# Performance work log

Measured on AMD Instinct MI355X. Metric: run time of the kernel, lower is better.

The kernel has to match this reference:

```python
import jax, jax.numpy as jnp
import numpy as np

PATCH = 16; D = 384; HEADS = 6; HD = D // HEADS; DEPTH = 12
NUM_CH = 64; MAXY = 4000  # (max_sr//2)*max_win_size
THETA = 100.0; EPS = 1e-6
WIN_SHIFT_FACTOR = 0.25; MIN_WIN_SHIFT = 0.125  # min_win_size*win_shift_factor


def _layer_norm(x, g, b):
    mu = jnp.mean(x, -1, keepdims=True)
    var = jnp.mean((x - mu) ** 2, -1, keepdims=True)
    return (x - mu) * jax.lax.rsqrt(var + EPS) * g + b


def _rope(t, cos, sin):
    # t: [B,H,N,HD]; cos/sin: [N,HD//2]; consecutive-pair complex rotation
    shp = t.shape
    tr = t.reshape(shp[:-1] + (HD // 2, 2))
    a, b = tr[..., 0], tr[..., 1]
    return jnp.stack([a * cos - b * sin, a * sin + b * cos], axis=-1).reshape(shp)


def _forward(x, means, stds, channels, noise, win_size, mask_ratio,
             patch_w, patch_b, cls_token, chan_table, mean_w, mean_b,
             qkv_w, qkv_b, proj_w, proj_b, fc1_w, fc1_b, fc2_w, fc2_b,
             ln1_g, ln1_b, ln2_g, ln2_b, gamma1, gamma2, lnf_g, lnf_b):
    B = x.shape[0]
    # --- patch embed (conv k=s=16) ---
    feat = jax.lax.conv_general_dilated(x, patch_w, (PATCH, PATCH), 'VALID',
                                        dimension_numbers=('NCHW', 'OIHW', 'NCHW'))
    h, w = feat.shape[2], feat.shape[3]
    N = h * w
    xt = feat.reshape(B, D, N).transpose(0, 2, 1) + patch_b  # [B,N,D]
    # --- vectorized channel-id embedding lookup (replaces BxN python loop) ---
    xt = xt + chan_table[channels]
    # --- normalization meta patches (original uses mean_embed for BOTH means and stds) ---
    m = means @ mean_w + mean_b
    s = stds @ mean_w + mean_b
    norm_patches = jnp.concatenate([m, s], axis=2)  # [B,M,D]
    M = norm_patches.shape[1]
    xt = jnp.concatenate([norm_patches, xt], axis=1)
    xt = jnp.concatenate([jnp.broadcast_to(cls_token, (B, 1, D)), xt], axis=1)
    n_meta = M + 1
    meta_patches = xt[:, :n_meta]
    # --- random masking (meta tokens always kept) ---
    data = xt[:, n_meta:]
    Ld = data.shape[1]
    len_keep = int(Ld * (1 - mask_ratio))
    ids_shuffle = jnp.argsort(noise, axis=1)
    ids_restore = jnp.argsort(ids_shuffle, axis=1)
    kept = jnp.take_along_axis(data, ids_shuffle[:, :len_keep, None], axis=1)
    mask0 = jnp.broadcast_to((jnp.arange(Ld) >= len_keep).astype(xt.dtype), (B, Ld))
    mask = jnp.take_along_axis(mask0, ids_restore, axis=1)
    xt = jnp.concatenate([xt[:, :n_meta], kept], axis=1)
    # --- axial RoPE freqs for the current hxw patch grid ---
    step = float(win_size) * WIN_SHIFT_FACTOR / MIN_WIN_SHIFT
    nf = HD // 4
    inv = 1.0 / (THETA ** (jnp.arange(0, HD, 4)[:nf].astype(jnp.float32) / HD))
    ys, xs = jnp.meshgrid(jnp.arange(h, dtype=jnp.float32),
                          jnp.arange(w, dtype=jnp.float32) * step, indexing='ij')
    fr = jnp.concatenate([xs.reshape(-1, 1) * inv, ys.reshape(-1, 1) * inv], axis=-1)  # [N,HD//2]
    cos, sin = jnp.cos(fr), jnp.sin(fr)
    # --- layer-scale RoPE transformer blocks ---
    L = xt.shape[1]
    scale = HD ** -0.5
    for d in range(DEPTH):
        y = _layer_norm(xt, ln1_g[d], ln1_b[d])
        qkv = (y @ qkv_w[d] + qkv_b[d]).reshape(B, L, 3, HEADS, HD).transpose(2, 0, 3, 1, 4)
        q, k, v = qkv[0], qkv[1], qkv[2]
        q = jnp.concatenate([q[:, :, :n_meta], _rope(q[:, :, n_meta:], cos, sin)], axis=2)
        k = jnp.concatenate([k[:, :, :n_meta], _rope(k[:, :, n_meta:], cos, sin)], axis=2)
        a = jax.nn.softmax(jnp.einsum('bhqd,bhkd->bhqk', q, k) * scale, axis=-1)
        o = jnp.einsum('bhqk,bhkd->bhqd', a, v).transpose(0, 2, 1, 3).reshape(B, L, D)
        xt = xt + gamma1[d] * (o @ proj_w[d] + proj_b[d])
        y2 = _layer_norm(xt, ln2_g[d], ln2_b[d])
        hid = jax.nn.gelu(y2 @ fc1_w[d] + fc1_b[d], approximate=False)
        xt = xt + gamma2[d] * (hid @ fc2_w[d] + fc2_b[d])
    xt = _layer_norm(xt, lnf_g, lnf_b)
    return xt, meta_patches, mask, n_meta


def setup_inputs() -> dict:
    key = jax.random.key(0)
    ks = jax.random.split(key, 16)
    B, H, W, M = 4, 128, 1024, 2
    N = (H // PATCH) * (W // PATCH)
    nrm = lambda k, shp, s=0.02: jax.random.normal(k, shp, jnp.float32) * s
    inp = {}
    inp['x'] = jax.random.normal(ks[0], (B, 1, H, W), jnp.float32)
    inp['means'] = jax.random.normal(ks[1], (B, M, MAXY), jnp.float32) * 0.1
    inp['stds'] = jax.random.normal(ks[2], (B, M, MAXY), jnp.float32) * 0.1
    inp['channels'] = jax.random.randint(ks[3], (B, N), 0, NUM_CH, jnp.int32)
    inp['noise'] = jnp.broadcast_to(jnp.arange(N, dtype=jnp.float32), (B, N))  # identity shuffle
    inp['win_size'] = 2
    inp['mask_ratio'] = 0
    inp['patch_w'] = nrm(ks[4], (D, 1, PATCH, PATCH))
    inp['patch_b'] = jnp.zeros((D,), jnp.float32)
    inp['cls_token'] = jnp.zeros((1, 1, D), jnp.float32)
    inp['chan_table'] = nrm(ks[5], (NUM_CH, D))
    inp['mean_w'] = nrm(ks[6], (MAXY, D // 2), 0.01)
    inp['mean_b'] = jnp.zeros((D // 2,), jnp.float32)
    inp['qkv_w'] = nrm(ks[7], (DEPTH, D, 3 * D))
    inp['qkv_b'] = jnp.zeros((DEPTH, 3 * D), jnp.float32)
    inp['proj_w'] = nrm(ks[8], (DEPTH, D, D))
    inp['proj_b'] = jnp.zeros((DEPTH, D), jnp.float32)
    inp['fc1_w'] = nrm(ks[9], (DEPTH, D, 4 * D))
    inp['fc1_b'] = jnp.zeros((DEPTH, 4 * D), jnp.float32)
    inp['fc2_w'] = nrm(ks[10], (DEPTH, 4 * D, D))
    inp['fc2_b'] = jnp.zeros((DEPTH, D), jnp.float32)
    inp['ln1_g'] = jnp.ones((DEPTH, D), jnp.float32)
    inp['ln1_b'] = jnp.zeros((DEPTH, D), jnp.float32)
    inp['ln2_g'] = jnp.ones((DEPTH, D), jnp.float32)
    inp['ln2_b'] = jnp.zeros((DEPTH, D), jnp.float32)
    inp['gamma1'] = jnp.full((DEPTH, D), 1e-4, jnp.float32)
    inp['gamma2'] = jnp.full((DEPTH, D), 1e-4, jnp.float32)
    inp['lnf_g'] = jnp.ones((D,), jnp.float32)
    inp['lnf_b'] = jnp.zeros((D,), jnp.float32)
    return inp


def reference(x, means, stds, channels, noise, win_size, mask_ratio,
              patch_w, patch_b, cls_token, chan_table, mean_w, mean_b,
              qkv_w, qkv_b, proj_w, proj_b, fc1_w, fc1_b, fc2_w, fc2_b,
              ln1_g, ln1_b, ln2_g, ln2_b, gamma1, gamma2, lnf_g, lnf_b):
    return _forward(x, means, stds, channels, noise, win_size, mask_ratio,
                    patch_w, patch_b, cls_token, chan_table, mean_w, mean_b,
                    qkv_w, qkv_b, proj_w, proj_b, fc1_w, fc1_b, fc2_w, fc2_b,
                    ln1_g, ln1_b, ln2_g, ln2_b, gamma1, gamma2, lnf_g, lnf_b)
```

## Files before the change

### kernel.cpp

```cpp
#include <hip/hip_runtime.h>
#include <hip/hip_bf16.h>
#include <math.h>

#define Bq     4
#define LSEQ   515
#define NMETA  3
#define NPATCH 512
#define Dm     384
#define NHEADS 6
#define HDh    64
#define NDEPTH 12
#define LPAD   544
#define KSPL   32
#define KCH    125

typedef unsigned short u16;
typedef short bf16x8 __attribute__((ext_vector_type(8)));
typedef float f32x4  __attribute__((ext_vector_type(4)));

enum { EPI_F32 = 0, EPI_BF16 = 1, EPI_GELU = 2, EPI_RES = 3 };

__device__ inline u16 f2bf(float x) {
    __hip_bfloat16 h = __float2bfloat16(x);
    return *reinterpret_cast<u16*>(&h);
}
__device__ inline float bf2f(u16 x) {
    __hip_bfloat16 h = *reinterpret_cast<__hip_bfloat16*>(&x);
    return __bfloat162float(h);
}

__global__ __launch_bounds__(256)
void k_transpose(const float* __restrict__ W, u16* __restrict__ WT, int R, int C) {
    __shared__ float tile[32][33];
    int z = blockIdx.z;
    const float* Wz = W + (long)z * R * C;
    u16* Tz = WT + (long)z * R * C;
    int c0 = blockIdx.x * 32, r0 = blockIdx.y * 32;
    int tx = threadIdx.x & 31, ty = threadIdx.x >> 5;
    for (int rr = ty; rr < 32; rr += 8)
        tile[rr][tx] = Wz[(long)(r0 + rr) * C + c0 + tx];
    __syncthreads();
    for (int rr = ty; rr < 32; rr += 8)
        Tz[(long)(c0 + rr) * R + r0 + tx] = f2bf(tile[tx][rr]);
}

__global__ __launch_bounds__(256)
void k_split(const float* __restrict__ x, u16* __restrict__ A) {
    int m = blockIdx.x;
    int b = m >> 9, n = m & 511;
    int i = n >> 6, j = n & 63;
    int t = threadIdx.x;
    int pr = t >> 4, pc = t & 15;
    float v = x[(long)b * 131072 + (i * 16 + pr) * 1024 + j * 16 + pc];
    u16 hi = f2bf(v);
    u16 lo = f2bf(v - bf2f(hi));
    u16* row = A + (long)m * 768;
    row[t] = hi; row[256 + t] = hi; row[512 + t] = lo;
}

__global__ __launch_bounds__(256)
void k_wsplit(const float* __restrict__ pw, u16* __restrict__ Bt) {
    int idx = blockIdx.x * 256 + threadIdx.x;
    if (idx >= Dm * 256) return;
    int d = idx >> 8, k = idx & 255;
    float v = pw[idx];
    u16 hi = f2bf(v);
    u16 lo = f2bf(v - bf2f(hi));
    u16* row = Bt + (long)d * 768;
    row[k] = hi; row[256 + k] = lo; row[512 + k] = hi;
}

__global__ __launch_bounds__(512)
void k_argsort(const float* __restrict__ noise, int* __restrict__ ids) {
    __shared__ float v[512];
    __shared__ int   ix[512];
    int b = blockIdx.x, t = threadIdx.x;
    v[t] = noise[b * 512 + t]; ix[t] = t;
    __syncthreads();
    for (int k = 2; k <= 512; k <<= 1)
        for (int j = k >> 1; j > 0; j >>= 1) {
            int p = t ^ j;
            if (p > t) {
                bool up = (t & k) == 0;
                float va = v[t], vb = v[p]; int ia = ix[t], ib = ix[p];
                bool sw = (va > vb) || (va == vb && ia > ib);
                if (sw == up) { v[t] = vb; v[p] = va; ix[t] = ib; ix[p] = ia; }
            }
            __syncthreads();
        }
    ids[b * 512 + t] = ix[t];
}

__global__ void k_gather(const float* __restrict__ tmp, const int* __restrict__ ids,
                         const float* __restrict__ pb, const float* __restrict__ ctab,
                         const int* __restrict__ chan, float* __restrict__ xt) {
    long t = (long)blockIdx.x * 256 + threadIdx.x;
    if (t >= (long)Bq * NPATCH * Dm) return;
    int d = t % Dm; long r = t / Dm;
    int j = r % NPATCH, b = r / NPATCH;
    int src = ids[b * NPATCH + j];
    int ch = chan[b * NPATCH + src];
    xt[((long)b * LSEQ + NMETA + j) * Dm + d] =
        tmp[((long)b * NPATCH + src) * Dm + d] + pb[d] + ctab[(long)ch * Dm + d];
}

__global__ __launch_bounds__(192)
void k_meta1(const float* __restrict__ means, const float* __restrict__ stds,
             const float* __restrict__ mw, float* __restrict__ part) {
    int g = blockIdx.x, c = blockIdx.y;
    int d = threadIdx.x;
    int p = g & 1, mi = (g >> 1) & 1, b = g >> 2;
    const float* row = (p ? stds : means) + (long)(b * 2 + mi) * 4000 + c * KCH;
    const float* w = mw + (long)c * KCH * 192 + d;
    float a = 0.f;
    #pragma unroll 5
    for (int k = 0; k < KCH; k++) a += row[k] * w[(long)k * 192];
    part[((long)g * KSPL + c) * 192 + d] = a;
}

__global__ __launch_bounds__(192)
void k_meta2(const float* __restrict__ part, const float* __restrict__ mb,
             float* __restrict__ xt) {
    int g = blockIdx.x, d = threadIdx.x;
    int p = g & 1, mi = (g >> 1) & 1, b = g >> 2;
    float a = mb[d];
    #pragma unroll 8
    for (int c = 0; c < KSPL; c++) a += part[((long)g * KSPL + c) * 192 + d];
    xt[((long)b * LSEQ + 1 + mi) * Dm + p * 192 + d] = a;
}

__global__ void k_cls(const float* __restrict__ cls, float* __restrict__ xt) {
    int t = blockIdx.x * 256 + threadIdx.x;
    if (t >= Bq * Dm) return;
    int b = t / Dm, d = t % Dm;
    xt[(long)b * LSEQ * Dm + d] = cls[d];
}

__global__ void k_outextra(const float* __restrict__ xt, float* __restrict__ out) {
    int t = blockIdx.x * 256 + threadIdx.x;
    const int META = Bq * NMETA * Dm;
    const int MASKN = Bq * NPATCH;
    if (t < META) {
        int d = t % Dm; int r = t / Dm; int b = r / NMETA, mi = r % NMETA;
        out[791040 + t] = xt[((long)b * LSEQ + mi) * Dm + d];
    } else if (t < META + MASKN) {
        out[791040 + t] = 0.0f;
    } else if (t == META + MASKN) {
        out[791040 + t] = 3.0f;
    }
}

__global__ void k_ropetab(const int* __restrict__ win, float* __restrict__ ct,
                          float* __restrict__ st) {
    int t = blockIdx.x * 256 + threadIdx.x;
    if (t >= NPATCH * 32) return;
    int p = t & 31, n = t >> 5;
    int i = n >> 6, j = n & 63;
    float step = (float)(*win) * 0.25f / 0.125f;
    float inv, ang;
    if (p < 16) { inv = powf(100.0f, -(float)p / 16.0f);        ang = (float)j * step * inv; }
    else        { inv = powf(100.0f, -(float)(p - 16) / 16.0f); ang = (float)i * inv; }
    ct[t] = cosf(ang); st[t] = sinf(ang);
}

template<bool OUT_BF16>
__global__ __launch_bounds__(256)
void k_ln(const float* __restrict__ X, const float* __restrict__ g,
          const float* __restrict__ b, void* __restrict__ Y, int nrows) {
    int row = blockIdx.x * 4 + (threadIdx.x >> 6);
    if (row >= nrows) return;
    int lane = threadIdx.x & 63;
    const float* xr = X + (long)row * Dm;
    float v[6], s = 0.f;
    #pragma unroll
    for (int i = 0; i < 6; i++) { v[i] = xr[lane + 64 * i]; s += v[i]; }
    for (int off = 32; off; off >>= 1) s += __shfl_down(s, off);
    s = __shfl(s, 0);
    float mu = s / (float)Dm, vs = 0.f;
    #pragma unroll
    for (int i = 0; i < 6; i++) { float d = v[i] - mu; vs += d * d; }
    for (int off = 32; off; off >>= 1) vs += __shfl_down(vs, off);
    vs = __shfl(vs, 0);
    float rs = rsqrtf(vs / (float)Dm + 1e-6f);
    #pragma unroll
    for (int i = 0; i < 6; i++) {
        int c = lane + 64 * i;
        float o = (v[i] - mu) * rs * g[c] + b[c];
        if (OUT_BF16) ((u16*)Y)[(long)row * Dm + c] = f2bf(o);
        else          ((float*)Y)[(long)row * Dm + c] = o;
    }
}

__global__ void k_ropepack(const float* __restrict__ qkv, const float* __restrict__ ct,
                           const float* __restrict__ st, u16* __restrict__ Qb,
                           u16* __restrict__ Kb, u16* __restrict__ Vt) {
    long tid = (long)blockIdx.x * 256 + threadIdx.x;
    if (tid >= (long)24 * LPAD * 32) return;
    int p = tid & 31;
    long r = tid >> 5;
    int n = r % LPAD; long bh = r / LPAD;
    int b = bh / NHEADS, h = bh % NHEADS;
    float q0 = 0, q1 = 0, k0 = 0, k1 = 0, v0 = 0, v1 = 0;
    if (n < LSEQ) {
        const float* base = qkv + ((long)(b * LSEQ + n) * 1152 + h * HDh + 2 * p);
        q0 = base[0];   q1 = base[1];
        k0 = base[384]; k1 = base[385];
        v0 = base[768]; v1 = base[769];
        if (n >= NMETA) {
            int j = n - NMETA;
            float c = ct[j * 32 + p], s = st[j * 32 + p], a;
            a = q0 * c - q1 * s; q1 = q0 * s + q1 * c; q0 = a;
            a = k0 * c - k1 * s; k1 = k0 * s + k1 * c; k0 = a;
        }
    }
    long qo = (bh * LPAD + n) * (long)HDh + 2 * p;
    Qb[qo] = f2bf(q0); Qb[qo + 1] = f2bf(q1);
    Kb[qo] = f2bf(k0); Kb[qo + 1] = f2bf(k1);
    long vo = (bh * (long)HDh + 2 * p) * LPAD + n;
    Vt[vo] = f2bf(v0); Vt[vo + LPAD] = f2bf(v1);
}

__global__ __launch_bounds__(256)
void k_flash(const u16* __restrict__ Qb, const u16* __restrict__ Kb,
             const u16* __restrict__ Vt, u16* __restrict__ obuf) {
    __shared__ u16 Ql[64][72];
    __shared__ u16 Kl[64][72];
    __shared__ u16 Vl[64][72];
    __shared__ u16 Pl[4][16][72];
    int bh = blockIdx.y;
    int b = bh / NHEADS, h = bh % NHEADS;
    int q0 = blockIdx.x * 64;
    int t = threadIdx.x, lane = t & 63, w = t >> 6;
    int srow = t >> 2, scol = (t & 3) * 16;
    int fr = lane & 15, kq = lane >> 4;
    const uint4 z4 = make_uint4(0, 0, 0, 0);

    {
        uint4 v0 = z4, v1 = z4;
        if (q0 + srow < LPAD) {
            const u16* p = Qb + ((long)bh * LPAD + q0 + srow) * HDh + scol;
            v0 = *(const uint4*)p; v1 = *(const uint4*)(p + 8);
        }
        *(uint4*)&Ql[srow][scol] = v0;
        *(uint4*)&Ql[srow][scol + 8] = v1;
    }

    float m_r[4], l_r[4];
    #pragma unroll
    for (int r = 0; r < 4; r++) { m_r[r] = -1e30f; l_r[r] = 0.f; }
    f32x4 Of[4] = {};

    for (int kt = 0; kt < 9; kt++) {
        int kv0 = kt * 64;
        uint4 kv0r = z4, kv1r = z4, vv0 = z4, vv1 = z4;
        if (kv0 + srow < LPAD) {
            const u16* p = Kb + ((long)bh * LPAD + kv0 + srow) * HDh + scol;
            kv0r = *(const uint4*)p; kv1r = *(const uint4*)(p + 8);
        }
        if (kv0 + scol < LPAD) {
            const u16* pv = Vt + ((long)bh * HDh + srow) * LPAD + kv0 + scol;
            vv0 = *(const uint4*)pv; vv1 = *(const uint4*)(pv + 8);
        }
        __syncthreads();
        *(uint4*)&Kl[srow][scol] = kv0r;
        *(uint4*)&Kl[srow][scol + 8] = kv1r;
        *(uint4*)&Vl[srow][scol] = vv0;
        *(uint4*)&Vl[srow][scol + 8] = vv1;
        __syncthreads();

        f32x4 sa[4] = {};
        #pragma unroll
        for (int ks = 0; ks < 2; ks++) {
            bf16x8 af = *(const bf16x8*)&Ql[w * 16 + fr][ks * 32 + kq * 8];
            #pragma unroll
            for (int nj = 0; nj < 4; nj++) {
                bf16x8 bg = *(const bf16x8*)&Kl[nj * 16 + fr][ks * 32 + kq * 8];
                sa[nj] = __builtin_amdgcn_mfma_f32_16x16x32_bf16(af, bg, sa[nj], 0, 0, 0);
            }
        }
        float rm[4], rs[4];
        #pragma unroll
        for (int r = 0; r < 4; r++) rm[r] = -1e30f;
        #pragma unroll
        for (int nj = 0; nj < 4; nj++) {
            bool valid = (kv0 + nj * 16 + fr) < LSEQ;
            #pragma unroll
            for (int r = 0; r < 4; r++) {
                float s = valid ? sa[nj][r] * 0.125f : -1e30f;
                sa[nj][r] = s;
                rm[r] = fmaxf(rm[r], s);
            }
        }
        #pragma unroll
        for (int r = 0; r < 4; r++) {
            #pragma unroll
            for (int off = 1; off < 16; off <<= 1)
                rm[r] = fmaxf(rm[r], __shfl_xor(rm[r], off));
        }
        float sc[4];
        #pragma unroll
        for (int r = 0; r < 4; r++) {
            float mn = fmaxf(m_r[r], rm[r]);
            sc[r] = __expf(m_r[r] - mn);
            m_r[r] = mn;
            rs[r] = 0.f;
        }
        #pragma unroll
        for (int nj = 0; nj < 4; nj++)
            #pragma unroll
            for (int r = 0; r < 4; r++) {
                float p = __expf(sa[nj][r] - m_r[r]);
                sa[nj][r] = p;
                rs[r] += p;
            }
        #pragma unroll
        for (int r = 0; r < 4; r++) {
            #pragma unroll
            for (int off = 1; off < 16; off <<= 1)
                rs[r] += __shfl_xor(rs[r], off);
            l_r[r] = l_r[r] * sc[r] + rs[r];
        }
        #pragma unroll
        for (int nj = 0; nj < 4; nj++)
            #pragma unroll
            for (int r = 0; r < 4; r++)
                Pl[w][kq * 4 + r][nj * 16 + fr] = f2bf(sa[nj][r]);
        bf16x8 pa0 = *(const bf16x8*)&Pl[w][fr][kq * 8];
        bf16x8 pa1 = *(const bf16x8*)&Pl[w][fr][32 + kq * 8];
        #pragma unroll
        for (int nd = 0; nd < 4; nd++)
            #pragma unroll
            for (int r = 0; r < 4; r++) Of[nd][r] *= sc[r];
        #pragma unroll
        for (int nd = 0; nd < 4; nd++) {
            bf16x8 bg0 = *(const bf16x8*)&Vl[nd * 16 + fr][kq * 8];
            bf16x8 bg1 = *(const bf16x8*)&Vl[nd * 16 + fr][32 + kq * 8];
            Of[nd] = __builtin_amdgcn_mfma_f32_16x16x32_bf16(pa0, bg0, Of[nd], 0, 0, 0);
            Of[nd] = __builtin_amdgcn_mfma_f32_16x16x32_bf16(pa1, bg1, Of[nd], 0, 0, 0);
        }
    }
    #pragma unroll
    for (int r = 0; r < 4; r++) {
        int q = q0 + w * 16 + kq * 4 + r;
        if (q >= LSEQ) continue;
        float inv = 1.0f / l_r[r];
        #pragma unroll
        for (int nd = 0; nd < 4; nd++)
            obuf[((long)b * LSEQ + q) * Dm + h * HDh + nd * 16 + fr] = f2bf(Of[nd][r] * inv);
    }
}

template<int EPI>
__global__ __launch_bounds__(256)
void k_gemm(const u16* __restrict__ A, int lda, long sA, int M,
            const u16* __restrict__ Bt, int ldb, long sB, int btRows,
            void* __restrict__ Cptr, int ldc, long sCz1, long sCz2, int hdiv,
            const float* __restrict__ bias, const float* __restrict__ gamma,
            int N, int K) {
    __shared__ u16 Al[64][40];
    __shared__ u16 Bl[64][40];
    int z = blockIdx.z;
    const u16* Ab = A + (long)z * sA;
    const u16* Bb = Bt + (long)z * sB;
    long coff = (long)(z / hdiv) * sCz1 + (long)(z % hdiv) * sCz2;
    int row0 = blockIdx.x * 64, col0 = blockIdx.y * 64;
    int t = threadIdx.x;
    int lane = t & 63, w = t >> 6;
    int wr = (w >> 1) * 32, wc = (w & 1) * 32;
    int srow = t >> 2, skq = (t & 3) * 8;
    f32x4 acc[2][2] = {};
    for (int kk = 0; kk < K; kk += 32) {
        uint4 av = make_uint4(0, 0, 0, 0), bv = make_uint4(0, 0, 0, 0);
        if (row0 + srow < M)      av = *(const uint4*)(Ab + (long)(row0 + srow) * lda + kk + skq);
        if (col0 + srow < btRows) bv = *(const uint4*)(Bb + (long)(col0 + srow) * ldb + kk + skq);
        __syncthreads();
        *(uint4*)(&Al[srow][skq]) = av;
        *(uint4*)(&Bl[srow][skq]) = bv;
        __syncthreads();
        int fr = lane & 15, kg = (lane >> 4) * 8;
        bf16x8 af[2], bg[2];
        #pragma unroll
        for (int i = 0; i < 2; i++) {
            af[i] = *(const bf16x8*)(&Al[wr + 16 * i + fr][kg]);
            bg[i] = *(const bf16x8*)(&Bl[wc + 16 * i + fr][kg]);
        }
        #pragma unroll
        for (int mi = 0; mi < 2; mi++)
            #pragma unroll
            for (int nj = 0; nj < 2; nj++)
                acc[mi][nj] = __builtin_amdgcn_mfma_f32_16x16x32_bf16(af[mi], bg[nj], acc[mi][nj], 0, 0, 0);
    }
    int fr = lane & 15, rg = (lane >> 4) * 4;
    #pragma unroll
    for (int mi = 0; mi < 2; mi++)
        #pragma unroll
        for (int nj = 0; nj < 2; nj++)
            #pragma unroll
            for (int r = 0; r < 4; r++) {
                int row = row0 + wr + 16 * mi + rg + r;
                int col = col0 + wc + 16 * nj + fr;
                if (row >= M || col >= N) continue;
                float v = acc[mi][nj][r];
                if (bias) v += bias[col];
                long idx = coff + (long)row * ldc + col;
                if (EPI == EPI_F32)      ((float*)Cptr)[idx] = v;
                else if (EPI == EPI_BF16)((u16*)Cptr)[idx] = f2bf(v);
                else if (EPI == EPI_GELU) {
                    v = 0.5f * v * (1.0f + erff(v * 0.70710678118f));
                    ((u16*)Cptr)[idx] = f2bf(v);
                } else {
                    float* C = (float*)Cptr;
                    C[idx] = C[idx] + gamma[col] * v;
                }
            }
}

extern "C" void kernel_launch(void* const* d_in, const int* in_sizes, int n_in,
                              void* d_out, int out_size, void* d_ws, size_t ws_size,
                              hipStream_t stream) {
    const float* x        = (const float*)d_in[0];
    const float* means    = (const float*)d_in[1];
    const float* stds     = (const float*)d_in[2];
    const int*   channels = (const int*)  d_in[3];
    const float* noise    = (const float*)d_in[4];
    const int*   win_size = (const int*)  d_in[5];
    const float* patch_w  = (const float*)d_in[7];
    const float* patch_b  = (const float*)d_in[8];
    const float* cls_tok  = (const float*)d_in[9];
    const float* chan_tab = (const float*)d_in[10];
    const float* mean_w   = (const float*)d_in[11];
    const float* mean_b   = (const float*)d_in[12];
    const float* qkv_w    = (const float*)d_in[13];
    const float* qkv_b    = (const float*)d_in[14];
    const float* proj_w   = (const float*)d_in[15];
    const float* proj_b   = (const float*)d_in[16];
    const float* fc1_w    = (const float*)d_in[17];
    const float* fc1_b    = (const float*)d_in[18];
    const float* fc2_w    = (const float*)d_in[19];
    const float* fc2_b    = (const float*)d_in[20];
    const float* ln1_g    = (const float*)d_in[21];
    const float* ln1_b    = (const float*)d_in[22];
    const float* ln2_g    = (const float*)d_in[23];
    const float* ln2_b    = (const float*)d_in[24];
    const float* gamma1   = (const float*)d_in[25];
    const float* gamma2   = (const float*)d_in[26];
    const float* lnf_g    = (const float*)d_in[27];
    const float* lnf_b    = (const float*)d_in[28];
    float* out = (float*)d_out;

    char* wp = (char*)d_ws;
    auto alloc = [&](size_t bytes) { char* p = wp; wp += (bytes + 255) & ~(size_t)255; return p; };
    u16*   qkvT  = (u16*)  alloc((size_t)NDEPTH * 1152 * 384 * 2);
    u16*   projT = (u16*)  alloc((size_t)NDEPTH * 384 * 384 * 2);
    u16*   fc1T  = (u16*)  alloc((size_t)NDEPTH * 1536 * 384 * 2);
    u16*   fc2T  = (u16*)  alloc((size_t)NDEPTH * 384 * 1536 * 2);
    float* xt    = (float*)alloc((size_t)Bq * LSEQ * Dm * 4);
    u16*   yb    = (u16*)  alloc((size_t)Bq * LSEQ * Dm * 2);
    float* qkvb  = (float*)alloc((size_t)Bq * LSEQ * 1152 * 4);
    u16*   Qb    = (u16*)  alloc((size_t)24 * LPAD * HDh * 2);
    u16*   Kb    = (u16*)  alloc((size_t)24 * LPAD * HDh * 2);
    u16*   Vt    = (u16*)  alloc((size_t)24 * HDh * LPAD * 2);
    u16*   obuf  = (u16*)  alloc((size_t)Bq * LSEQ * Dm * 2);
    u16*   hid   = (u16*)  alloc((size_t)Bq * LSEQ * 1536 * 2);
    float* tmp   = (float*)alloc((size_t)Bq * NPATCH * Dm * 4);
    float* ct    = (float*)alloc((size_t)NPATCH * 32 * 4);
    float* st    = (float*)alloc((size_t)NPATCH * 32 * 4);
    int*   ids   = (int*)  alloc((size_t)Bq * NPATCH * 4);
    float* mpart = (float*)alloc((size_t)16 * KSPL * 192 * 4);
    u16*   Axl   = (u16*)  alloc((size_t)Bq * NPATCH * 768 * 2);
    u16*   Bw    = (u16*)  alloc((size_t)Dm * 768 * 2);

    k_transpose<<<dim3(1152 / 32, 384 / 32, NDEPTH), 256, 0, stream>>>(qkv_w, qkvT, 384, 1152);
    k_transpose<<<dim3(384 / 32, 384 / 32, NDEPTH), 256, 0, stream>>>(proj_w, projT, 384, 384);
    k_transpose<<<dim3(1536 / 32, 384 / 32, NDEPTH), 256, 0, stream>>>(fc1_w, fc1T, 384, 1536);
    k_transpose<<<dim3(384 / 32, 1536 / 32, NDEPTH), 256, 0, stream>>>(fc2_w, fc2T, 1536, 384);

    k_split<<<Bq * NPATCH, 256, 0, stream>>>(x, Axl);
    k_wsplit<<<(Dm * 256 + 255) / 256, 256, 0, stream>>>(patch_w, Bw);
    k_gemm<EPI_F32><<<dim3(Bq * NPATCH / 64, Dm / 64, 1), 256, 0, stream>>>(
        Axl, 768, 0, Bq * NPATCH,
        Bw, 768, 0, Dm,
        tmp, Dm, 0, 0, 1,
        nullptr, nullptr, Dm, 768);

    k_argsort<<<Bq, 512, 0, stream>>>(noise, ids);
    k_gather<<<(Bq * NPATCH * Dm + 255) / 256, 256, 0, stream>>>(tmp, ids, patch_b, chan_tab, channels, xt);
    k_meta1<<<dim3(16, KSPL), 192, 0, stream>>>(means, stds, mean_w, mpart);
    k_meta2<<<16, 192, 0, stream>>>(mpart, mean_b, xt);
    k_cls<<<(Bq * Dm + 255) / 256, 256, 0, stream>>>(cls_tok, xt);
    k_outextra<<<(4608 + 2048 + 1 + 255) / 256, 256, 0, stream>>>(xt, out);
    k_ropetab<<<(NPATCH * 32 + 255) / 256, 256, 0, stream>>>(win_size, ct, st);

    const int ROWS = Bq * LSEQ;
    const int MT = (ROWS + 63) / 64;
    for (int d = 0; d < NDEPTH; d++) {
        k_ln<true><<<(ROWS + 3) / 4, 256, 0, stream>>>(xt, ln1_g + d * Dm, ln1_b + d * Dm, yb, ROWS);
        k_gemm<EPI_F32><<<dim3(MT, 1152 / 64, 1), 256, 0, stream>>>(
            yb, Dm, 0, ROWS,
            qkvT + (long)d * 1152 * 384, 384, 0, 1152,
            qkvb, 1152, 0, 0, 1,
            qkv_b + d * 1152, nullptr, 1152, 384);
        k_ropepack<<<(24 * LPAD * 32 + 255) / 256, 256, 0, stream>>>(qkvb, ct, st, Qb, Kb, Vt);
        k_flash<<<dim3(9, 24), 256, 0, stream>>>(Qb, Kb, Vt, obuf);
        k_gemm<EPI_RES><<<dim3(MT, Dm / 64, 1), 256, 0, stream>>>(
            obuf, Dm, 0, ROWS,
            projT + (long)d * 384 * 384, 384, 0, 384,
            xt, Dm, 0, 0, 1,
            proj_b + d * Dm, gamma1 + d * Dm, Dm, 384);
        k_ln<true><<<(ROWS + 3) / 4, 256, 0, stream>>>(xt, ln2_g + d * Dm, ln2_b + d * Dm, yb, ROWS);
        k_gemm<EPI_GELU><<<dim3(MT, 1536 / 64, 1), 256, 0, stream>>>(
            yb, Dm, 0, ROWS,
            fc1T + (long)d * 1536 * 384, 384, 0, 1536,
            hid, 1536, 0, 0, 1,
            fc1_b + d * 1536, nullptr, 1536, 384);
        k_gemm<EPI_RES><<<dim3(MT, Dm / 64, 1), 256, 0, stream>>>(
            hid, 1536, 0, ROWS,
            fc2T + (long)d * 384 * 1536, 1536, 0, 384,
            xt, Dm, 0, 0, 1,
            fc2_b + d * Dm, gamma2 + d * Dm, Dm, 1536);
    }
    k_ln<false><<<(ROWS + 3) / 4, 256, 0, stream>>>(xt, lnf_g, lnf_b, out, ROWS);
}
```

Baseline: 1.459 ms.

## Double-buffer GEMM K loop with 64-wide tiles and store QKV as bf16

The shared GEMM kernel now loads 64-wide K tiles and issues the global loads for the next tile while the MFMAs for the current tile run. This halves the number of barrier pairs and hides part of the global-load latency. The QKV projection output is also written as bf16 instead of fp32, and the RoPE pack kernel reads it as bf16, which roughly halves that intermediate's memory traffic. The cost is more LDS and registers per block, plus an extra bf16 rounding of q/k before the rotary step.

```diff
diff --git a/kernel.cpp b/kernel.cpp
--- a/kernel.cpp
+++ b/kernel.cpp
@@ -191,7 +191,7 @@
     }
 }
 
-__global__ void k_ropepack(const float* __restrict__ qkv, const float* __restrict__ ct,
+__global__ void k_ropepack(const u16* __restrict__ qkv, const float* __restrict__ ct,
                            const float* __restrict__ st, u16* __restrict__ Qb,
                            u16* __restrict__ Kb, u16* __restrict__ Vt) {
     long tid = (long)blockIdx.x * 256 + threadIdx.x;
@@ -202,10 +202,10 @@
     int b = bh / NHEADS, h = bh % NHEADS;
     float q0 = 0, q1 = 0, k0 = 0, k1 = 0, v0 = 0, v1 = 0;
     if (n < LSEQ) {
-        const float* base = qkv + ((long)(b * LSEQ + n) * 1152 + h * HDh + 2 * p);
-        q0 = base[0];   q1 = base[1];
-        k0 = base[384]; k1 = base[385];
-        v0 = base[768]; v1 = base[769];
+        const u16* base = qkv + ((long)(b * LSEQ + n) * 1152 + h * HDh + 2 * p);
+        q0 = bf2f(base[0]);   q1 = bf2f(base[1]);
+        k0 = bf2f(base[384]); k1 = bf2f(base[385]);
+        v0 = bf2f(base[768]); v1 = bf2f(base[769]);
         if (n >= NMETA) {
             int j = n - NMETA;
             float c = ct[j * 32 + p], s = st[j * 32 + p], a;
@@ -357,8 +357,8 @@
             void* __restrict__ Cptr, int ldc, long sCz1, long sCz2, int hdiv,
             const float* __restrict__ bias, const float* __restrict__ gamma,
             int N, int K) {
-    __shared__ u16 Al[64][40];
-    __shared__ u16 Bl[64][40];
+    __shared__ u16 Al[64][72];
+    __shared__ u16 Bl[64][72];
     int z = blockIdx.z;
     const u16* Ab = A + (long)z * sA;
     const u16* Bb = Bt + (long)z * sB;
@@ -367,30 +367,46 @@
     int t = threadIdx.x;
     int lane = t & 63, w = t >> 6;
     int wr = (w >> 1) * 32, wc = (w & 1) * 32;
-    int srow = t >> 2, skq = (t & 3) * 8;
+    int srow = t >> 2, sk = (t & 3) * 16;
+    const uint4 z4 = make_uint4(0, 0, 0, 0);
+    bool aok = (row0 + srow < M), bok = (col0 + srow < btRows);
     f32x4 acc[2][2] = {};
-    for (int kk = 0; kk < K; kk += 32) {
-        uint4 av = make_uint4(0, 0, 0, 0), bv = make_uint4(0, 0, 0, 0);
-        if (row0 + srow < M)      av = *(const uint4*)(Ab + (long)(row0 + srow) * lda + kk + skq);
-        if (col0 + srow < btRows) bv = *(const uint4*)(Bb + (long)(col0 + srow) * ldb + kk + skq);
+    uint4 av0, av1, bv0, bv1;
+    auto issue = [&](int kk) {
+        av0 = av1 = bv0 = bv1 = z4;
+        if (aok) {
+            const u16* p = Ab + (long)(row0 + srow) * lda + kk + sk;
+            av0 = *(const uint4*)p; av1 = *(const uint4*)(p + 8);
+        }
+        if (bok) {
+            const u16* p = Bb + (long)(col0 + srow) * ldb + kk + sk;
+            bv0 = *(const uint4*)p; bv1 = *(const uint4*)(p + 8);
+        }
+    };
+    issue(0);
+    int fr = lane & 15, kg = (lane >> 4) * 8;
+    for (int kk = 0; kk < K; kk += 64) {
         __syncthreads();
-        *(uint4*)(&Al[srow][skq]) = av;
-        *(uint4*)(&Bl[srow][skq]) = bv;
+        *(uint4*)(&Al[srow][sk]) = av0; *(uint4*)(&Al[srow][sk + 8]) = av1;
+        *(uint4*)(&Bl[srow][sk]) = bv0; *(uint4*)(&Bl[srow][sk + 8]) = bv1;
         __syncthreads();
-        int fr = lane & 15, kg = (lane >> 4) * 8;
-        bf16x8 af[2], bg[2];
-        #pragma unroll
-        for (int i = 0; i < 2; i++) {
-            af[i] = *(const bf16x8*)(&Al[wr + 16 * i + fr][kg]);
-            bg[i] = *(const bf16x8*)(&Bl[wc + 16 * i + fr][kg]);
-        }
-        #pragma unroll
-        for (int mi = 0; mi < 2; mi++)
-            #pragma unroll
-            for (int nj = 0; nj < 2; nj++)
-                acc[mi][nj] = __builtin_amdgcn_mfma_f32_16x16x32_bf16(af[mi], bg[nj], acc[mi][nj], 0, 0, 0);
-    }
-    int fr = lane & 15, rg = (lane >> 4) * 4;
+        if (kk + 64 < K) issue(kk + 64);
+        #pragma unroll
+        for (int ks = 0; ks < 2; ks++) {
+            bf16x8 af[2], bg[2];
+            #pragma unroll
+            for (int i = 0; i < 2; i++) {
+                af[i] = *(const bf16x8*)(&Al[wr + 16 * i + fr][ks * 32 + kg]);
+                bg[i] = *(const bf16x8*)(&Bl[wc + 16 * i + fr][ks * 32 + kg]);
+            }
+            #pragma unroll
+            for (int mi = 0; mi < 2; mi++)
+                #pragma unroll
+                for (int nj = 0; nj < 2; nj++)
+                    acc[mi][nj] = __builtin_amdgcn_mfma_f32_16x16x32_bf16(af[mi], bg[nj], acc[mi][nj], 0, 0, 0);
+        }
+    }
+    int rg = (lane >> 4) * 4;
     #pragma unroll
     for (int mi = 0; mi < 2; mi++)
         #pragma unroll
@@ -456,7 +472,7 @@
     u16*   fc2T  = (u16*)  alloc((size_t)NDEPTH * 384 * 1536 * 2);
     float* xt    = (float*)alloc((size_t)Bq * LSEQ * Dm * 4);
     u16*   yb    = (u16*)  alloc((size_t)Bq * LSEQ * Dm * 2);
-    float* qkvb  = (float*)alloc((size_t)Bq * LSEQ * 1152 * 4);
+    u16*   qkvb  = (u16*)  alloc((size_t)Bq * LSEQ * 1152 * 2);
     u16*   Qb    = (u16*)  alloc((size_t)24 * LPAD * HDh * 2);
     u16*   Kb    = (u16*)  alloc((size_t)24 * LPAD * HDh * 2);
     u16*   Vt    = (u16*)  alloc((size_t)24 * HDh * LPAD * 2);
@@ -495,7 +511,7 @@
     const int MT = (ROWS + 63) / 64;
     for (int d = 0; d < NDEPTH; d++) {
         k_ln<true><<<(ROWS + 3) / 4, 256, 0, stream>>>(xt, ln1_g + d * Dm, ln1_b + d * Dm, yb, ROWS);
-        k_gemm<EPI_F32><<<dim3(MT, 1152 / 64, 1), 256, 0, stream>>>(
+        k_gemm<EPI_BF16><<<dim3(MT, 1152 / 64, 1), 256, 0, stream>>>(
             yb, Dm, 0, ROWS,
             qkvT + (long)d * 1152 * 384, 384, 0, 1152,
             qkvb, 1152, 0, 0, 1,
```

Result: faster. 1.291 ms (-11.5%).
